# Kernel optimization log

Measured on AMD Instinct MI355X. Metric: run time of the kernel, lower is better.

## Reference

```python
import jax, jax.numpy as jnp
import numpy as np

EPS = 1e-5
GROUPS = 32

def group_norm(x, w, b):
    B, C, H, W = x.shape
    g = GROUPS
    xr = x.reshape(B, g, C // g, H * W)
    mean = xr.mean(axis=(2, 3), keepdims=True)
    var = xr.var(axis=(2, 3), keepdims=True)
    h = ((xr - mean) / jnp.sqrt(var + EPS)).reshape(B, C, H, W)
    return h * w[None, :, None, None] + b[None, :, None, None]

def setup_inputs() -> dict:
    key = jax.random.key(0)
    ks = jax.random.split(key, 7)
    B, C, H, W = 8, 256, 64, 64
    d = C // 8  # 32
    x = jax.random.normal(ks[0], (B, C, H, W), dtype=jnp.float32)
    norm_w = 1.0 + 0.1 * jax.random.normal(ks[1], (C,), dtype=jnp.float32)
    norm_b = 0.1 * jax.random.normal(ks[2], (C,), dtype=jnp.float32)
    s = 1.0 / np.sqrt(C)
    Wq = jax.random.normal(ks[3], (d, C), dtype=jnp.float32) * s
    Wk = jax.random.normal(ks[4], (d, C), dtype=jnp.float32) * s
    Wv = jax.random.normal(ks[5], (C, C), dtype=jnp.float32) * s
    Wproj = jax.random.normal(ks[6], (C, C), dtype=jnp.float32) * s
    gamma = jnp.full((1,), 0.5, dtype=jnp.float32)  # torch init is 0; nonzero so attention path contributes
    return {"x": x, "norm_w": norm_w, "norm_b": norm_b, "Wq": Wq, "Wk": Wk,
            "Wv": Wv, "Wproj": Wproj, "gamma": gamma}

def reference(x, norm_w, norm_b, Wq, Wk, Wv, Wproj, gamma):
    B, C, H, W = x.shape
    N = H * W
    h = group_norm(x, norm_w, norm_b)           # (B,C,H,W)
    hf = h.reshape(B, C, N)                      # flatten spatial
    d = Wq.shape[0]
    q = jnp.einsum('dc,bcn->bnd', Wq, hf)        # (B,N,d)
    k = jnp.einsum('dc,bcn->bdn', Wk, hf)        # (B,d,N)
    v = jnp.einsum('oc,bcn->bno', Wv, hf)        # (B,N,C)
    scale = d ** (-0.5)
    attn = jax.nn.softmax(jnp.einsum('bnd,bdm->bnm', q, k) * scale, axis=-1)  # (B,N,N)
    out = jnp.einsum('bnm,bmo->bno', attn, v)    # (B,N,C)
    out = out.transpose(0, 2, 1).reshape(B, C, H, W)
    proj = jnp.einsum('oc,bchw->bohw', Wproj, out)
    return x + gamma[0] * proj
```

## Files before the change

kernel.cpp:

```cpp
#include <hip/hip_runtime.h>
#include <cstdint>


typedef __bf16 bf16x8 __attribute__((ext_vector_type(8)));
typedef float f32x4 __attribute__((ext_vector_type(4)));
typedef float f32x16 __attribute__((ext_vector_type(16)));
typedef unsigned int u32x4 __attribute__((ext_vector_type(4)));
typedef unsigned short u16x4 __attribute__((ext_vector_type(4)));
typedef unsigned short u16x8 __attribute__((ext_vector_type(8)));

#define DEVI __device__ __forceinline__

DEVI unsigned short f2bf(float f) {
    __bf16 h = (__bf16)f;
    return __builtin_bit_cast(unsigned short, h);
}
DEVI float bf2f(unsigned short u) {
    unsigned int x = ((unsigned int)u) << 16;
    return __builtin_bit_cast(float, x);
}

DEVI f32x4 mfma16(bf16x8 a, bf16x8 b, f32x4 c) {
    return __builtin_amdgcn_mfma_f32_16x16x32_bf16(a, b, c, 0, 0, 0);
}
DEVI f32x16 mfma32(bf16x8 a, bf16x8 b, f32x16 c) {
    return __builtin_amdgcn_mfma_f32_32x32x16_bf16(a, b, c, 0, 0, 0);
}

DEVI void glds16(const unsigned short* g, unsigned short* l) {
    const __attribute__((address_space(1))) unsigned int* gp =
        reinterpret_cast<const __attribute__((address_space(1))) unsigned int*>(
            reinterpret_cast<uintptr_t>(g));
    __attribute__((address_space(3))) unsigned int* lp =
        reinterpret_cast<__attribute__((address_space(3))) unsigned int*>(
            reinterpret_cast<uintptr_t>(l));
    __builtin_amdgcn_global_load_lds(gp, lp, 16, 0, 0);
}

DEVI void barrier_raw() {
    asm volatile("" ::: "memory");
    __builtin_amdgcn_s_barrier();
    asm volatile("" ::: "memory");
}
DEVI void wait_vm0() {
    __builtin_amdgcn_s_waitcnt(0x3F70);
}

#define QSCALE 0.2550663133f
#define MFIX   12.0f

__global__ __launch_bounds__(1024) void k_gnorm(
        const float* __restrict__ x, const float* __restrict__ gw,
        const float* __restrict__ gb, unsigned short* __restrict__ ht) {
    int bg = blockIdx.x;
    int b = bg >> 5, g = bg & 31;
    const float* xb = x + ((size_t)(b * 256 + g * 8)) * 4096;
    int t = threadIdx.x;
    int n0 = t * 4;
    f32x4 cv[8];
    #pragma unroll
    for (int c = 0; c < 8; c++) cv[c] = *(const f32x4*)(xb + c * 4096 + n0);
    float s1 = 0.f, s2 = 0.f;
    #pragma unroll
    for (int c = 0; c < 8; c++) {
        #pragma unroll
        for (int j = 0; j < 4; j++) { s1 += cv[c][j]; s2 += cv[c][j] * cv[c][j]; }
    }
    #pragma unroll
    for (int off = 1; off < 64; off <<= 1) {
        s1 += __shfl_xor(s1, off);
        s2 += __shfl_xor(s2, off);
    }
    __shared__ float red[34];
    int wv_ = t >> 6;
    if ((t & 63) == 0) { red[wv_ * 2] = s1; red[wv_ * 2 + 1] = s2; }
    __syncthreads();
    if (t == 0) {
        float a = 0.f, q = 0.f;
        #pragma unroll
        for (int i = 0; i < 16; i++) { a += red[i * 2]; q += red[i * 2 + 1]; }
        float mean = a * (1.f / 32768.f);
        float var = q * (1.f / 32768.f) - mean * mean;
        red[32] = mean; red[33] = rsqrtf(var + 1e-5f);
    }
    __syncthreads();
    float mean = red[32], rstd = red[33];
    float wv8[8], bv8[8];
    #pragma unroll
    for (int c = 0; c < 8; c++) { wv8[c] = gw[g * 8 + c] * rstd; bv8[c] = gb[g * 8 + c] - mean * rstd * gw[g * 8 + c]; }
    #pragma unroll
    for (int j = 0; j < 4; j++) {
        u16x8 pk;
        #pragma unroll
        for (int c = 0; c < 8; c++) pk[c] = f2bf(cv[c][j] * wv8[c] + bv8[c]);
        *(u16x8*)(&ht[((size_t)(b * 4096 + n0 + j)) * 256 + g * 8]) = pk;
    }
}

template <int EPI>
__global__ __launch_bounds__(256) void k_gemm(
        const unsigned short* __restrict__ A, void* __restrict__ outp,
        const float* __restrict__ xres, const float* __restrict__ gamma, int ldout,
        const float* __restrict__ wqf, const float* __restrict__ wkf,
        const float* __restrict__ wvf, void* __restrict__ outp2) {
    __shared__ unsigned short lA[128 * 72];
    __shared__ unsigned short lB[64 * 72];
    int t = threadIdx.x;
    int m0 = blockIdx.x * 128, n0 = blockIdx.y * 64;
    if (EPI == 3) {
        if (blockIdx.y == 0) n0 = 0;
        else n0 = (blockIdx.y - 1) * 64;
    }
    int w = t >> 6, lane = t & 63, l15 = lane & 15, quad = lane >> 4;
    f32x4 z4 = {0.f, 0.f, 0.f, 0.f};
    f32x4 acc[2][4];
    #pragma unroll
    for (int i = 0; i < 2; i++)
        #pragma unroll
        for (int j = 0; j < 4; j++) acc[i][j] = z4;

    auto ldB8 = [&](int row, int gc) -> u16x8 {
        const float* src;
        float sc = 1.f;
        if (EPI == 3) {
            if (blockIdx.y == 0) {
                if (row < 32) { src = wqf + (size_t)row * 256 + gc; sc = QSCALE; }
                else          { src = wkf + (size_t)(row - 32) * 256 + gc; }
            } else {
                src = wvf + (size_t)(n0 + row) * 256 + gc;
            }
        } else {
            src = wvf + (size_t)(n0 + row) * 256 + gc;
        }
        f32x4 a = *(const f32x4*)src;
        f32x4 b2 = *(const f32x4*)(src + 4);
        u16x8 r;
        #pragma unroll
        for (int j = 0; j < 4; j++) { r[j] = f2bf(a[j] * sc); r[4 + j] = f2bf(b2[j] * sc); }
        return r;
    };

    for (int kb = 0; kb < 4; kb++) {
        #pragma unroll
        for (int i = 0; i < 4; i++) {
            int ch = i * 256 + t;
            int row = ch >> 3, col = (ch & 7) * 8;
            u32x4 v = *(const u32x4*)(A + (size_t)(m0 + row) * 256 + kb * 64 + col);
            *(u32x4*)(&lA[row * 72 + col]) = v;
        }
        #pragma unroll
        for (int i = 0; i < 2; i++) {
            int ch = i * 256 + t;
            int row = ch >> 3, col = (ch & 7) * 8;
            u16x8 v = ldB8(row, kb * 64 + col);
            *(u16x8*)(&lB[row * 72 + col]) = v;
        }
        __syncthreads();
        #pragma unroll
        for (int ks = 0; ks < 2; ks++) {
            bf16x8 af[2], bfr[4];
            #pragma unroll
            for (int fr = 0; fr < 2; fr++)
                af[fr] = *(const bf16x8*)(&lA[(w * 32 + fr * 16 + l15) * 72 + ks * 32 + quad * 8]);
            #pragma unroll
            for (int fn = 0; fn < 4; fn++)
                bfr[fn] = *(const bf16x8*)(&lB[(fn * 16 + l15) * 72 + ks * 32 + quad * 8]);
            #pragma unroll
            for (int fr = 0; fr < 2; fr++)
                #pragma unroll
                for (int fn = 0; fn < 4; fn++)
                    acc[fr][fn] = mfma16(af[fr], bfr[fn], acc[fr][fn]);
        }
        __syncthreads();
    }

    bool epi0 = (EPI == 3 && blockIdx.y == 0);
    bool epi1 = (EPI == 3 && blockIdx.y != 0);
    if (epi0) {
        unsigned short* out = (unsigned short*)outp;
        #pragma unroll
        for (int fr = 0; fr < 2; fr++)
            #pragma unroll
            for (int fn = 0; fn < 4; fn++)
                #pragma unroll
                for (int r = 0; r < 4; r++) {
                    int m = m0 + w * 32 + fr * 16 + quad * 4 + r;
                    int n = n0 + fn * 16 + l15;
                    out[(size_t)m * ldout + n] = f2bf(acc[fr][fn][r]);
                }
    } else if (epi1) {
        unsigned short* out = (unsigned short*)outp2;
        int b = m0 >> 12, nb = (m0 & 4095) + w * 32;
        int swq = ((quad & 1) << 1) | (quad >> 1);
        #pragma unroll
        for (int fr = 0; fr < 2; fr++)
            #pragma unroll
            for (int fn = 0; fn < 4; fn++) {
                int o = n0 + fn * 16 + l15;
                int n = nb + fr * 16 + swq * 4;
                u16x4 pk;
                #pragma unroll
                for (int r = 0; r < 4; r++) pk[r] = f2bf(acc[fr][fn][r]);
                *(u16x4*)(&out[(((size_t)(b * 256 + o)) << 12) + n]) = pk;
            }
    } else {
        float* out = (float*)outp;
        float gm = gamma[0];
        int b = m0 >> 12, nb = (m0 & 4095) + w * 32;
        #pragma unroll
        for (int fr = 0; fr < 2; fr++)
            #pragma unroll
            for (int fn = 0; fn < 4; fn++) {
                int o = n0 + fn * 16 + l15;
                int n = nb + fr * 16 + quad * 4;
                size_t base = (((size_t)(b * 256 + o)) << 12) + n;
                f32x4 xv = *(const f32x4*)(xres + base);
                f32x4 ov;
                #pragma unroll
                for (int r = 0; r < 4; r++) ov[r] = xv[r] + gm * acc[fr][fn][r];
                *(f32x4*)(out + base) = ov;
            }
    }
}

__global__ __launch_bounds__(256, 2) void k_flash(
        const unsigned short* __restrict__ QK, const unsigned short* __restrict__ Vt,
        unsigned short* __restrict__ Oa) {
    __shared__ __align__(16) char smem[73728];
    int id = blockIdx.x;
    int b = id & 7;
    int qblk = id >> 3;
    int t = threadIdx.x, w = t >> 6, ln = t & 63;
    int l31 = ln & 31, h = ln >> 5;
    int qh = w >> 1, kh = w & 1;

    const unsigned short* qrow = QK + ((size_t)(b * 4096 + qblk * 64 + qh * 32 + l31)) * 64;
    bf16x8 qb0 = *(const bf16x8*)(qrow + h * 8);
    bf16x8 qb1 = *(const bf16x8*)(qrow + 16 + h * 8);

    int cgK = (ln & 3) ^ ((ln >> 2) & 3) ^ ((ln >> 4) & 3);
    const unsigned short* gK = QK + ((size_t)(b * 4096 + w * 16 + (ln >> 2))) * 64 + 32 + cgK * 8;
    int vc8 = (ln & 7) ^ ((ln >> 3) & 7);
    const unsigned short* gV = Vt + (((size_t)(b * 256 + w * 64 + (ln >> 3))) << 12) + vc8 * 8;

    unsigned short* lK0 = (unsigned short*)smem;
    unsigned short* lV0 = (unsigned short*)(smem + 4096);
    unsigned short* lK1 = (unsigned short*)(smem + 36864);
    unsigned short* lV1 = (unsigned short*)(smem + 40960);
    unsigned short* sK0 = lK0 + w * 512;
    unsigned short* sV0 = lV0 + w * 4096;
    unsigned short* sK1 = lK1 + w * 512;
    unsigned short* sV1 = lV1 + w * 4096;

    f32x16 z16;
    #pragma unroll
    for (int i = 0; i < 16; i++) z16[i] = 0.f;
    f32x16 minit;
    #pragma unroll
    for (int i = 0; i < 16; i++) minit[i] = -MFIX;
    f32x16 Oacc[8];
    #pragma unroll
    for (int i = 0; i < 8; i++) Oacc[i] = z16;
    float lsum = 0.f;

    int gl = (l31 & 3) ^ ((l31 >> 2) & 3);
    const unsigned short* kf0p0 = lK0 + (kh * 32 + l31) * 32 + ((0 + h) ^ gl) * 8;
    const unsigned short* kf1p0 = lK0 + (kh * 32 + l31) * 32 + ((2 + h) ^ gl) * 8;
    const unsigned short* kf0p1 = lK1 + (kh * 32 + l31) * 32 + ((0 + h) ^ gl) * 8;
    const unsigned short* kf1p1 = lK1 + (kh * 32 + l31) * 32 + ((2 + h) ^ gl) * 8;
    int slotA = ((kh * 4 + 0 * 2 + h) ^ (ln & 7)) * 8;
    int slotB = ((kh * 4 + 1 * 2 + h) ^ (ln & 7)) * 8;

    auto stage = [&](int kn, unsigned short* sK, unsigned short* sV) {
        glds16(gK + (size_t)kn * 4096, sK);
        #pragma unroll
        for (int j = 0; j < 8; j++)
            glds16(gV + ((size_t)j * 8 << 12) + kn * 64, sV + j * 512);
    };

    auto compute = [&](const unsigned short* kf0p, const unsigned short* kf1p,
                       const unsigned short* lV) {
        bf16x8 kf0 = *(const bf16x8*)kf0p;
        bf16x8 kf1 = *(const bf16x8*)kf1p;
        f32x16 St = mfma32(kf0, qb0, minit);
        St = mfma32(kf1, qb1, St);
        u16x8 p0u, p1u;
        float s = 0.f;
        #pragma unroll
        for (int j = 0; j < 8; j++) {
            float e0 = __builtin_amdgcn_exp2f(St[j]);
            float e1 = __builtin_amdgcn_exp2f(St[8 + j]);
            s += e0 + e1;
            p0u[j] = f2bf(e0);
            p1u[j] = f2bf(e1);
        }
        lsum += s;
        bf16x8 pa0 = __builtin_bit_cast(bf16x8, p0u);
        bf16x8 pa1 = __builtin_bit_cast(bf16x8, p1u);
        __builtin_amdgcn_s_setprio(1);
        #pragma unroll
        for (int ot = 0; ot < 8; ot++) {
            bf16x8 vf = *(const bf16x8*)(lV + (ot * 32 + l31) * 64 + slotA);
            Oacc[ot] = mfma32(pa0, vf, Oacc[ot]);
        }
        #pragma unroll
        for (int ot = 0; ot < 8; ot++) {
            bf16x8 vf = *(const bf16x8*)(lV + (ot * 32 + l31) * 64 + slotB);
            Oacc[ot] = mfma32(pa1, vf, Oacc[ot]);
        }
        __builtin_amdgcn_s_setprio(0);
    };

    stage(0, sK0, sV0);
    for (int kt = 0; kt < 64; kt += 2) {
        wait_vm0();
        barrier_raw();
        stage(kt + 1, sK1, sV1);
        compute(kf0p0, kf1p0, lV0);
        wait_vm0();
        barrier_raw();
        if (kt + 2 < 64) stage(kt + 2, sK0, sV0);
        compute(kf0p1, kf1p1, lV1);
    }
    lsum += __shfl_xor(lsum, 32);
    __syncthreads();

    float* sf = (float*)smem;
    int lbase = (kh ? 8192 : 8256) + qh * 32 + l31;
    sf[lbase] = lsum;
    if (kh == 1) {
        #pragma unroll
        for (int ot = 0; ot < 8; ot++)
            #pragma unroll
            for (int rg = 0; rg < 2; rg++) {
                u16x8 pk;
                #pragma unroll
                for (int j = 0; j < 8; j++) pk[j] = f2bf(Oacc[ot][rg * 8 + j]);
                *(u16x8*)(smem + qh * 16384 + ot * 2048 + rg * 1024 + ln * 16) = pk;
            }
    }
    __syncthreads();
    if (kh == 0) {
        float rl[16];
        #pragma unroll
        for (int r = 0; r < 16; r++) {
            int row = (r & 3) + 8 * (r >> 2) + 4 * h;
            float l = sf[8192 + qh * 32 + row] + sf[8256 + qh * 32 + row];
            rl[r] = 1.f / l;
        }
        size_t rb = (size_t)(b * 4096 + qblk * 64 + qh * 32);
        #pragma unroll
        for (int ot = 0; ot < 8; ot++)
            #pragma unroll
            for (int rg = 0; rg < 2; rg++) {
                u16x8 pk = *(const u16x8*)(smem + qh * 16384 + ot * 2048 + rg * 1024 + ln * 16);
                #pragma unroll
                for (int j = 0; j < 8; j++) {
                    int r = rg * 8 + j;
                    float val = (Oacc[ot][r] + bf2f(pk[j])) * rl[r];
                    int row = (r & 3) + 8 * (r >> 2) + 4 * h;
                    Oa[(rb + row) * 256 + ot * 32 + l31] = f2bf(val);
                }
            }
    }
}

extern "C" void kernel_launch(void* const* d_in, const int* in_sizes, int n_in,
                              void* d_out, int out_size, void* d_ws, size_t ws_size,
                              hipStream_t stream) {
    const float* x  = (const float*)d_in[0];
    const float* nw = (const float*)d_in[1];
    const float* nb = (const float*)d_in[2];
    const float* wq = (const float*)d_in[3];
    const float* wk = (const float*)d_in[4];
    const float* wv = (const float*)d_in[5];
    const float* wp = (const float*)d_in[6];
    const float* gm = (const float*)d_in[7];

    char* p = (char*)d_ws;
    unsigned short* ht  = (unsigned short*)p; p += (size_t)32768 * 256 * 2;
    unsigned short* qk  = (unsigned short*)p; p += (size_t)32768 * 64 * 2;
    unsigned short* vt  = (unsigned short*)p; p += (size_t)8 * 256 * 4096 * 2;
    unsigned short* oa  = (unsigned short*)p; p += (size_t)32768 * 256 * 2;

    k_gnorm<<<dim3(256), dim3(1024), 0, stream>>>(x, nw, nb, ht);
    k_gemm<3><<<dim3(256, 5), dim3(256), 0, stream>>>(ht, (void*)qk, nullptr, nullptr, 64, wq, wk, wv, (void*)vt);
    k_flash<<<dim3(512), dim3(256), 0, stream>>>(qk, vt, oa);
    k_gemm<2><<<dim3(256, 4), dim3(256), 0, stream>>>(oa, d_out, x, gm, 0, nullptr, nullptr, wp, nullptr);
}
```

Before: 230.0 us.

## Split flash attention output channels across two blocks to raise occupancy

Each flash block now computes only half of the 256 value channels, selected by a new oh index, and the grid doubles to 1024 blocks. This halves the V staging in LDS, the accumulator registers and the LDS footprint, so launch bounds can allow 3 blocks per CU. The cost is that QK^T and the softmax exponentials are recomputed twice, once per channel half, and K tiles are loaded twice.

```diff
diff --git a/kernel.cpp b/kernel.cpp
--- a/kernel.cpp
+++ b/kernel.cpp
@@ -223,13 +223,14 @@
     }
 }
 
-__global__ __launch_bounds__(256, 2) void k_flash(
+__global__ __launch_bounds__(256, 3) void k_flash(
         const unsigned short* __restrict__ QK, const unsigned short* __restrict__ Vt,
         unsigned short* __restrict__ Oa) {
-    __shared__ __align__(16) char smem[73728];
+    __shared__ __align__(16) char smem[40960];
     int id = blockIdx.x;
     int b = id & 7;
-    int qblk = id >> 3;
+    int r3 = id >> 3;
+    int oh = r3 & 1, qblk = r3 >> 1;
     int t = threadIdx.x, w = t >> 6, ln = t & 63;
     int l31 = ln & 31, h = ln >> 5;
     int qh = w >> 1, kh = w & 1;
@@ -241,16 +242,16 @@
     int cgK = (ln & 3) ^ ((ln >> 2) & 3) ^ ((ln >> 4) & 3);
     const unsigned short* gK = QK + ((size_t)(b * 4096 + w * 16 + (ln >> 2))) * 64 + 32 + cgK * 8;
     int vc8 = (ln & 7) ^ ((ln >> 3) & 7);
-    const unsigned short* gV = Vt + (((size_t)(b * 256 + w * 64 + (ln >> 3))) << 12) + vc8 * 8;
+    const unsigned short* gV = Vt + (((size_t)(b * 256 + oh * 128 + w * 32 + (ln >> 3))) << 12) + vc8 * 8;
 
     unsigned short* lK0 = (unsigned short*)smem;
     unsigned short* lV0 = (unsigned short*)(smem + 4096);
-    unsigned short* lK1 = (unsigned short*)(smem + 36864);
-    unsigned short* lV1 = (unsigned short*)(smem + 40960);
+    unsigned short* lK1 = (unsigned short*)(smem + 20480);
+    unsigned short* lV1 = (unsigned short*)(smem + 24576);
     unsigned short* sK0 = lK0 + w * 512;
-    unsigned short* sV0 = lV0 + w * 4096;
+    unsigned short* sV0 = lV0 + w * 2048;
     unsigned short* sK1 = lK1 + w * 512;
-    unsigned short* sV1 = lV1 + w * 4096;
+    unsigned short* sV1 = lV1 + w * 2048;
 
     f32x16 z16;
     #pragma unroll
@@ -258,9 +259,9 @@
     f32x16 minit;
     #pragma unroll
     for (int i = 0; i < 16; i++) minit[i] = -MFIX;
-    f32x16 Oacc[8];
-    #pragma unroll
-    for (int i = 0; i < 8; i++) Oacc[i] = z16;
+    f32x16 Oacc[4];
+    #pragma unroll
+    for (int i = 0; i < 4; i++) Oacc[i] = z16;
     float lsum = 0.f;
 
     int gl = (l31 & 3) ^ ((l31 >> 2) & 3);
@@ -274,7 +275,7 @@
     auto stage = [&](int kn, unsigned short* sK, unsigned short* sV) {
         glds16(gK + (size_t)kn * 4096, sK);
         #pragma unroll
-        for (int j = 0; j < 8; j++)
+        for (int j = 0; j < 4; j++)
             glds16(gV + ((size_t)j * 8 << 12) + kn * 64, sV + j * 512);
     };
 
@@ -299,14 +300,14 @@
         bf16x8 pa1 = __builtin_bit_cast(bf16x8, p1u);
         __builtin_amdgcn_s_setprio(1);
         #pragma unroll
-        for (int ot = 0; ot < 8; ot++) {
-            bf16x8 vf = *(const bf16x8*)(lV + (ot * 32 + l31) * 64 + slotA);
-            Oacc[ot] = mfma32(pa0, vf, Oacc[ot]);
-        }
-        #pragma unroll
-        for (int ot = 0; ot < 8; ot++) {
-            bf16x8 vf = *(const bf16x8*)(lV + (ot * 32 + l31) * 64 + slotB);
-            Oacc[ot] = mfma32(pa1, vf, Oacc[ot]);
+        for (int nt = 0; nt < 4; nt++) {
+            bf16x8 vf = *(const bf16x8*)(lV + (nt * 32 + l31) * 64 + slotA);
+            Oacc[nt] = mfma32(pa0, vf, Oacc[nt]);
+        }
+        #pragma unroll
+        for (int nt = 0; nt < 4; nt++) {
+            bf16x8 vf = *(const bf16x8*)(lV + (nt * 32 + l31) * 64 + slotB);
+            Oacc[nt] = mfma32(pa1, vf, Oacc[nt]);
         }
         __builtin_amdgcn_s_setprio(0);
     };
@@ -330,13 +331,13 @@
     sf[lbase] = lsum;
     if (kh == 1) {
         #pragma unroll
-        for (int ot = 0; ot < 8; ot++)
+        for (int nt = 0; nt < 4; nt++)
             #pragma unroll
             for (int rg = 0; rg < 2; rg++) {
                 u16x8 pk;
                 #pragma unroll
-                for (int j = 0; j < 8; j++) pk[j] = f2bf(Oacc[ot][rg * 8 + j]);
-                *(u16x8*)(smem + qh * 16384 + ot * 2048 + rg * 1024 + ln * 16) = pk;
+                for (int j = 0; j < 8; j++) pk[j] = f2bf(Oacc[nt][rg * 8 + j]);
+                *(u16x8*)(smem + qh * 8192 + nt * 2048 + rg * 1024 + ln * 16) = pk;
             }
     }
     __syncthreads();
@@ -350,16 +351,16 @@
         }
         size_t rb = (size_t)(b * 4096 + qblk * 64 + qh * 32);
         #pragma unroll
-        for (int ot = 0; ot < 8; ot++)
+        for (int nt = 0; nt < 4; nt++)
             #pragma unroll
             for (int rg = 0; rg < 2; rg++) {
-                u16x8 pk = *(const u16x8*)(smem + qh * 16384 + ot * 2048 + rg * 1024 + ln * 16);
+                u16x8 pk = *(const u16x8*)(smem + qh * 8192 + nt * 2048 + rg * 1024 + ln * 16);
                 #pragma unroll
                 for (int j = 0; j < 8; j++) {
                     int r = rg * 8 + j;
-                    float val = (Oacc[ot][r] + bf2f(pk[j])) * rl[r];
+                    float val = (Oacc[nt][r] + bf2f(pk[j])) * rl[r];
                     int row = (r & 3) + 8 * (r >> 2) + 4 * h;
-                    Oa[(rb + row) * 256 + ot * 32 + l31] = f2bf(val);
+                    Oa[(rb + row) * 256 + oh * 128 + nt * 32 + l31] = f2bf(val);
                 }
             }
     }
@@ -385,6 +386,6 @@
 
     k_gnorm<<<dim3(256), dim3(1024), 0, stream>>>(x, nw, nb, ht);
     k_gemm<3><<<dim3(256, 5), dim3(256), 0, stream>>>(ht, (void*)qk, nullptr, nullptr, 64, wq, wk, wv, (void*)vt);
-    k_flash<<<dim3(512), dim3(256), 0, stream>>>(qk, vt, oa);
+    k_flash<<<dim3(1024), dim3(256), 0, stream>>>(qk, vt, oa);
     k_gemm<2><<<dim3(256, 4), dim3(256), 0, stream>>>(oa, d_out, x, gm, 0, nullptr, nullptr, wp, nullptr);
 }
```

New measurement: 246.9 us. 1.07x slower.
